# Kernel tuning notes

Hardware: AMD Instinct MI355X
Metric: run time of the kernel (lower is better)

The kernel has to match this reference:

```python
import jax, jax.numpy as jnp
import numpy as np

NUM_HEADS = 16
CAPACITY = 512
ROPE_BASE = 10000.0

def _rope_factor(positions, dim):
    # freqs = exp(linspace(0,-1,dim//2) * log(base)), shape (dim//2,)
    freqs = jnp.exp(jnp.linspace(0.0, -1.0, dim // 2) * jnp.log(jnp.float32(ROPE_BASE)))
    angles = positions[..., None] * freqs            # (..., seq, dim//2)
    return jnp.concatenate([jnp.sin(angles), jnp.cos(angles)], axis=-1)  # (..., seq, dim)

def setup_inputs() -> dict:
    key = jax.random.key(0)
    ks = jax.random.split(key, 6)
    B, Sq, Skv, D = 4, 4096, 4096, 1024
    return {
        "query_seq": jax.random.normal(ks[0], (B, Sq, D), jnp.float32),
        "value_seq": jax.random.normal(ks[1], (B, Skv, D), jnp.float32),
        "router_w": jax.random.normal(ks[2], (1, D), jnp.float32) * 0.02,
        "q_w": jax.random.normal(ks[3], (D, D), jnp.float32) * 0.02,
        "kv_w": jax.random.normal(ks[4], (2 * D, D), jnp.float32) * 0.02,
        "out_w": jax.random.normal(ks[5], (D, D), jnp.float32) * 0.02,
    }

def reference(query_seq, value_seq, router_w, q_w, kv_w, out_w):
    B, Sq, D = query_seq.shape
    Skv = value_seq.shape[1]
    H, C = NUM_HEADS, CAPACITY
    d = D // H

    # router + top-k capacity selection over the sequence dim
    rw = jnp.einsum("bsd,od->bs", query_seq, router_w).astype(jnp.float32)  # (B,Sq)
    top_w, top_idx = jax.lax.top_k(rw, C)                                   # (B,C)

    # gather selected queries
    resampled = jnp.take_along_axis(query_seq, top_idx[:, :, None], axis=1)  # (B,C,D)

    q = jnp.einsum("bcd,ed->bce", resampled, q_w)        # (B,C,H*d)
    kv = jnp.einsum("bsd,ed->bse", value_seq, kv_w)      # (B,Skv,2*H*d)
    k, v = jnp.split(kv, 2, axis=-1)

    q = q.reshape(B, C, H, d).transpose(0, 2, 1, 3)      # (B,H,C,d)
    k = k.reshape(B, Skv, H, d).transpose(0, 2, 1, 3)    # (B,H,Skv,d)
    v = v.reshape(B, Skv, H, d).transpose(0, 2, 1, 3)

    # RoPE-style elementwise modulation (faithful to source: x * cat(sin, cos))
    q_pos = top_idx.astype(jnp.float32)[:, None, :]      # (B,1,C)
    q = q * _rope_factor(q_pos, d)                       # (B,H,C,d)
    k_pos = jnp.arange(Skv, dtype=jnp.float32)[None, :]  # (1,Skv)
    k = k * _rope_factor(k_pos, d)[None]                 # broadcast over (B,H)

    # SDPA
    scores = jnp.einsum("bhcd,bhsd->bhcs", q, k) / jnp.sqrt(jnp.float32(d))
    att = jnp.einsum("bhcs,bhsd->bhcd", jax.nn.softmax(scores, axis=-1), v)

    att = att.transpose(0, 2, 1, 3).reshape(B, C, H * d)  # (B,C,D)
    att = jnp.einsum("bce,de->bcd", att, out_w)           # (B,C,D)

    # weighted scatter back to full sequence
    src = att * top_w[:, :, None]
    out = jnp.zeros_like(query_seq).at[jnp.arange(B)[:, None], top_idx].set(src)
    return out
```

## Files before the change

### kernel.cpp

```cpp
#include <hip/hip_runtime.h>
#include <hip/hip_bf16.h>

#define B_  4
#define SQ  4096
#define SKV 4096
#define DM  1024
#define NH  16
#define HD  64
#define CAP 512

#define ASPLIT 4
#define KVPER  (SKV / ASPLIT)
#define AITERS (KVPER / 64)

typedef __attribute__((ext_vector_type(8))) short    short8;
typedef __attribute__((ext_vector_type(8))) __bf16   bf16v8;
typedef __attribute__((ext_vector_type(4))) float    f32x4;
typedef __attribute__((ext_vector_type(4))) unsigned short ushort4v;
typedef __attribute__((ext_vector_type(4))) unsigned int   uint4v;

static __device__ __forceinline__ unsigned short f2bf(float f) {
    unsigned u = __float_as_uint(f);
    u += 0x7FFFu + ((u >> 16) & 1u);
    return (unsigned short)(u >> 16);
}

static __device__ __forceinline__ f32x4 mfma_bf16(short8 a, short8 b, f32x4 c) {
    return __builtin_amdgcn_mfma_f32_16x16x32_bf16(
        __builtin_bit_cast(bf16v8, a), __builtin_bit_cast(bf16v8, b), c, 0, 0, 0);
}

#define GLD16(gp, lp)                                                              \
    __builtin_amdgcn_global_load_lds(                                              \
        (__attribute__((address_space(1))) void*)(gp),                             \
        (__attribute__((address_space(3))) void*)(lp), 16, 0, 0)

__global__ void __launch_bounds__(256) k_convert(const float* __restrict__ in,
                                                 unsigned short* __restrict__ out) {
    size_t i = (size_t)blockIdx.x * 256 + threadIdx.x;
    float4 f = ((const float4*)in)[i];
    ushort4v o = { f2bf(f.x), f2bf(f.y), f2bf(f.z), f2bf(f.w) };
    ((ushort4v*)out)[i] = o;
}

__global__ void __launch_bounds__(256) k_rope(float* __restrict__ tab) {
    int g = blockIdx.x * 256 + threadIdx.x;
    int pos = g >> 6, i = g & 63, j = i & 31;
    float freq = expf(-(float)j * (logf(10000.0f) / 31.0f));
    float ang  = (float)pos * freq;
    tab[g] = (i < 32) ? sinf(ang) : cosf(ang);
}

__global__ void __launch_bounds__(256) k_router(const float* __restrict__ q,
                                                const float* __restrict__ wv,
                                                float* __restrict__ rw) {
    int row  = blockIdx.x * 4 + (threadIdx.x >> 6);
    int lane = threadIdx.x & 63;
    const float* p  = q  + (size_t)row * DM + lane * 16;
    const float* wp = wv + lane * 16;
    float s = 0.f;
#pragma unroll
    for (int j = 0; j < 4; j++) {
        float4 a = ((const float4*)p)[j];
        float4 b = ((const float4*)wp)[j];
        s += a.x * b.x + a.y * b.y + a.z * b.z + a.w * b.w;
    }
#pragma unroll
    for (int m = 32; m > 0; m >>= 1) s += __shfl_xor(s, m, 64);
    if (lane == 0) rw[row] = s;
}

__global__ void __launch_bounds__(1024) k_topk(const float* __restrict__ rw,
                                               int* __restrict__ sel,
                                               float* __restrict__ selw) {
    __shared__ unsigned long long keys[4096];
    int b = blockIdx.x, t = threadIdx.x;
    for (int i = t; i < 4096; i += 1024) {
        float v = rw[b * 4096 + i];
        unsigned u = __float_as_uint(v);
        u = (u & 0x80000000u) ? ~u : (u | 0x80000000u);
        keys[i] = ((unsigned long long)(~u) << 32) | (unsigned)i;
    }
    __syncthreads();
    for (int k = 2; k <= 4096; k <<= 1)
        for (int j = k >> 1; j > 0; j >>= 1) {
            for (int i = t; i < 4096; i += 1024) {
                int ixj = i ^ j;
                if (ixj > i) {
                    bool up = ((i & k) == 0);
                    unsigned long long a = keys[i], c = keys[ixj];
                    if ((a > c) == up) { keys[i] = c; keys[ixj] = a; }
                }
            }
            __syncthreads();
        }
    for (int i = t; i < 512; i += 1024) {
        unsigned idx = (unsigned)(keys[i] & 0xFFFFFFFFu);
        sel[b * 512 + i]  = (int)idx;
        selw[b * 512 + i] = rw[b * 4096 + idx];
    }
}

__global__ void __launch_bounds__(256) k_gather(const float* __restrict__ q,
                                                const int* __restrict__ sel,
                                                unsigned short* __restrict__ out) {
    int row = blockIdx.x;
    int b = row >> 9;
    int s = sel[row];
    const float4* src = (const float4*)(q + ((size_t)b * SQ + s) * DM);
    ushort4v* dst = (ushort4v*)(out + (size_t)row * DM);
    float4 f = src[threadIdx.x];
    ushort4v o = { f2bf(f.x), f2bf(f.y), f2bf(f.z), f2bf(f.w) };
    dst[threadIdx.x] = o;
}

template <int MODE, int BN>
__global__ void __launch_bounds__(256) k_gemm(
    const unsigned short* __restrict__ A,
    const unsigned short* __restrict__ Bw,
    int M, int N, int K,
    const float* __restrict__ rope_tab,
    const int* __restrict__ sel,
    const float* __restrict__ selw,
    unsigned short* __restrict__ ok,
    unsigned short* __restrict__ ov,
    unsigned short* __restrict__ obf,
    float* __restrict__ of) {
    constexpr int TN = BN / 32;
    __shared__ unsigned short lA[128 * 32];
    __shared__ unsigned short lB[BN * 32];
    const int tid = threadIdx.x;
    const int w = tid >> 6, lane = tid & 63, quad = lane >> 4, l16 = lane & 15;
    const int wr = w >> 1, wc = w & 1;
    const int mBase = blockIdx.y * 128;
    const int nBase = blockIdx.x * BN + (MODE == 3 ? 1024 : 0);

    f32x4 acc[4][TN] = {};

    for (int k0 = 0; k0 < K; k0 += 32) {
#pragma unroll
        for (int is = 0; is < 2; is++) {
            int slot = is * 256 + tid;
            int row = slot >> 2, sc = slot & 3;
            int kc = (sc - (row >> 1)) & 3;
            const char* ga = (const char*)A + (((size_t)(mBase + row) * K) + k0 + kc * 8) * 2;
            GLD16(ga, (char*)lA + slot * 16);
        }
#pragma unroll
        for (int is = 0; is < BN / 64; is++) {
            int slot = is * 256 + tid;
            int row = slot >> 2, sc = slot & 3;
            int kc = (sc - (row >> 1)) & 3;
            const char* gb = (const char*)Bw + (((size_t)(nBase + row) * K) + k0 + kc * 8) * 2;
            GLD16(gb, (char*)lB + slot * 16);
        }
        __syncthreads();
        short8 af[4], bfr[TN];
#pragma unroll
        for (int t = 0; t < 4; t++) {
            int r = wr * 64 + t * 16 + l16;
            af[t] = *(const short8*)&lA[r * 32 + (((quad + (r >> 1)) & 3) * 8)];
        }
#pragma unroll
        for (int t = 0; t < TN; t++) {
            int r = wc * (BN / 2) + t * 16 + l16;
            bfr[t] = *(const short8*)&lB[r * 32 + (((quad + (r >> 1)) & 3) * 8)];
        }
#pragma unroll
        for (int tm = 0; tm < 4; tm++)
#pragma unroll
            for (int tn = 0; tn < TN; tn++) {
                if constexpr (MODE == 3)
                    acc[tm][tn] = mfma_bf16(bfr[tn], af[tm], acc[tm][tn]);
                else
                    acc[tm][tn] = mfma_bf16(af[tm], bfr[tn], acc[tm][tn]);
            }
        __syncthreads();
    }

#pragma unroll
    for (int tm = 0; tm < 4; tm++) {
#pragma unroll
        for (int tn = 0; tn < TN; tn++) {
#pragma unroll
            for (int r = 0; r < 4; r++) {
                float v = acc[tm][tn][r];
                if constexpr (MODE == 3) {
                    int n = nBase + wc * (BN / 2) + tn * 16 + quad * 4 + r;
                    int m = mBase + wr * 64 + tm * 16 + l16;
                    int e = n - 1024, h = e >> 6, i = e & 63;
                    int b = m >> 12, s = m & 4095;
                    ov[(((size_t)(b * NH + h) * HD) + i) * SKV + s] = f2bf(v);
                } else {
                    int m = mBase + wr * 64 + tm * 16 + quad * 4 + r;
                    int n = nBase + wc * (BN / 2) + tn * 16 + l16;
                    if constexpr (MODE == 0) {
                        int b = m >> 12, s = m & 4095;
                        int h = n >> 6, i = n & 63;
                        v *= rope_tab[(s << 6) | i];
                        ok[(((size_t)(b * NH + h) * SKV) + s) * HD + i] = f2bf(v);
                    } else if constexpr (MODE == 1) {
                        int b = m >> 9, c = m & 511;
                        int h = n >> 6, i = n & 63;
                        float rp = rope_tab[(sel[m] << 6) | i];
                        obf[(((size_t)(b * NH + h) * CAP) + c) * HD + i] =
                            f2bf(v * rp * 0.18033688011112042f);
                    } else {
                        int b = m >> 9;
                        int s = sel[m];
                        of[(((size_t)b * SQ) + s) * DM + n] = v * selw[m];
                    }
                }
            }
        }
    }
}

__global__ void __launch_bounds__(256) k_attention(
    const unsigned short* __restrict__ Q,
    const unsigned short* __restrict__ Kg,
    const unsigned short* __restrict__ Vt,
    float* __restrict__ Opart,
    float* __restrict__ Lpart) {
    __shared__ unsigned short lK[64 * 72];
    __shared__ unsigned short lV[64 * 72];
    const int bh = blockIdx.y, z = blockIdx.z;
    const int tid = threadIdx.x, w = tid >> 6, lane = tid & 63;
    const int quad = lane >> 4, l16 = lane & 15;
    const int qb = blockIdx.x * 128 + w * 32;
    const int base = z * KVPER;

    short8 qf[2][2];
#pragma unroll
    for (int rt = 0; rt < 2; rt++) {
        const unsigned short* qp = Q + ((size_t)bh * CAP + qb + rt * 16 + l16) * HD + quad * 8;
        qf[rt][0] = *(const short8*)qp;
        qf[rt][1] = *(const short8*)(qp + 32);
    }

    const unsigned short* kb = Kg + (size_t)bh * SKV * HD;
    const unsigned short* vb = Vt + (size_t)bh * HD * SKV;
    const int sr = tid >> 2, sp = tid & 3;

    f32x4 o[2][4] = {};
    f32x4 lsum[2] = {};
    short8 ones = (short8)0x3F80;

    short8 rk0, rk1, rv0, rv1;
    {
        const short8* srck = (const short8*)(kb + (size_t)(base + sr) * HD + sp * 16);
        rk0 = srck[0]; rk1 = srck[1];
        const short8* srcv = (const short8*)(vb + (size_t)sr * SKV + base + sp * 16);
        rv0 = srcv[0]; rv1 = srcv[1];
    }

    for (int it = 0; it < AITERS; it++) {
        __syncthreads();
        *(short8*)&lK[sr * 72 + sp * 16]     = rk0;
        *(short8*)&lK[sr * 72 + sp * 16 + 8] = rk1;
        *(short8*)&lV[sr * 72 + sp * 16]     = rv0;
        *(short8*)&lV[sr * 72 + sp * 16 + 8] = rv1;
        if (it + 1 < AITERS) {
            int s0 = base + (it + 1) * 64;
            const short8* srck = (const short8*)(kb + (size_t)(s0 + sr) * HD + sp * 16);
            rk0 = srck[0]; rk1 = srck[1];
            const short8* srcv = (const short8*)(vb + (size_t)sr * SKV + s0 + sp * 16);
            rv0 = srcv[0]; rv1 = srcv[1];
        }
        __syncthreads();

        f32x4 sc[2][4] = {};
#pragma unroll
        for (int tn = 0; tn < 4; tn++) {
            short8 kf0 = *(const short8*)&lK[(tn * 16 + l16) * 72 + quad * 8];
            short8 kf1 = *(const short8*)&lK[(tn * 16 + l16) * 72 + 32 + quad * 8];
#pragma unroll
            for (int rt = 0; rt < 2; rt++) {
                sc[rt][tn] = mfma_bf16(kf0, qf[rt][0], sc[rt][tn]);
                sc[rt][tn] = mfma_bf16(kf1, qf[rt][1], sc[rt][tn]);
            }
        }
#pragma unroll
        for (int rt = 0; rt < 2; rt++)
#pragma unroll
            for (int tn = 0; tn < 4; tn++)
#pragma unroll
                for (int r = 0; r < 4; r++)
                    sc[rt][tn][r] = exp2f(fminf(sc[rt][tn][r], 86.f));

        short8 pa[2][2];
#pragma unroll
        for (int rt = 0; rt < 2; rt++)
#pragma unroll
            for (int kc = 0; kc < 2; kc++) {
                uint4v wv;
#pragma unroll
                for (int t = 0; t < 4; t++) {
                    unsigned pk;
                    asm("v_cvt_pk_bf16_f32 %0, %1, %2"
                        : "=v"(pk)
                        : "v"(sc[rt][kc * 2 + (t >> 1)][(t & 1) * 2]),
                          "v"(sc[rt][kc * 2 + (t >> 1)][(t & 1) * 2 + 1]));
                    wv[t] = pk;
                }
                pa[rt][kc] = __builtin_bit_cast(short8, wv);
            }

#pragma unroll
        for (int kc = 0; kc < 2; kc++) {
            lsum[0] = mfma_bf16(pa[0][kc], ones, lsum[0]);
            lsum[1] = mfma_bf16(pa[1][kc], ones, lsum[1]);
#pragma unroll
            for (int tn = 0; tn < 4; tn++) {
                const unsigned short* vrow = &lV[(size_t)(tn * 16 + l16) * 72];
                uint2 g0 = *(const uint2*)(vrow + kc * 32 + quad * 4);
                uint2 g1 = *(const uint2*)(vrow + kc * 32 + 16 + quad * 4);
                uint4v wv = { g0.x, g0.y, g1.x, g1.y };
                short8 vf = __builtin_bit_cast(short8, wv);
                o[0][tn] = mfma_bf16(pa[0][kc], vf, o[0][tn]);
                o[1][tn] = mfma_bf16(pa[1][kc], vf, o[1][tn]);
            }
        }
    }

    float* Ob = Opart + (((size_t)(z * 64 + bh)) * CAP + qb) * HD;
#pragma unroll
    for (int rt = 0; rt < 2; rt++)
#pragma unroll
        for (int tn = 0; tn < 4; tn++)
#pragma unroll
            for (int r = 0; r < 4; r++)
                Ob[(size_t)(rt * 16 + quad * 4 + r) * HD + tn * 16 + l16] = o[rt][tn][r];
    if (l16 == 0) {
#pragma unroll
        for (int rt = 0; rt < 2; rt++)
#pragma unroll
            for (int r = 0; r < 4; r++)
                Lpart[((size_t)(z * 64 + bh)) * CAP + qb + rt * 16 + quad * 4 + r] = lsum[rt][r];
    }
}

__global__ void __launch_bounds__(256) k_combine(
    const float* __restrict__ Opart, const float* __restrict__ Lpart,
    unsigned short* __restrict__ att) {
    int g = blockIdx.x * 256 + threadIdx.x;
    int dall = g & 1023, c = (g >> 10) & 511, b = g >> 19;
    int h = dall >> 6, dd = dall & 63;
    int bh = b * NH + h;
    float os = 0.f, ls = 0.f;
#pragma unroll
    for (int p = 0; p < ASPLIT; p++) {
        os += Opart[(((size_t)(p * 64 + bh)) * CAP + c) * HD + dd];
        ls += Lpart[((size_t)(p * 64 + bh)) * CAP + c];
    }
    att[g] = f2bf(os / ls);
}

extern "C" void kernel_launch(void* const* d_in, const int* in_sizes, int n_in,
                              void* d_out, int out_size, void* d_ws, size_t ws_size,
                              hipStream_t stream) {
    const float* query    = (const float*)d_in[0];
    const float* value    = (const float*)d_in[1];
    const float* router_w = (const float*)d_in[2];
    const float* q_w      = (const float*)d_in[3];
    const float* kv_w     = (const float*)d_in[4];
    const float* out_w    = (const float*)d_in[5];
    float* out = (float*)d_out;

    char* p = (char*)d_ws;
    unsigned short* value_bf = (unsigned short*)p; p += (size_t)B_ * SKV * DM * 2;
    unsigned short* kvw_bf   = (unsigned short*)p; p += (size_t)2 * DM * DM * 2;
    unsigned short* qw_bf    = (unsigned short*)p; p += (size_t)DM * DM * 2;
    unsigned short* ow_bf    = (unsigned short*)p; p += (size_t)DM * DM * 2;
    unsigned short* res_bf   = (unsigned short*)p; p += (size_t)B_ * CAP * DM * 2;
    unsigned short* q_attn   = (unsigned short*)p; p += (size_t)B_ * CAP * DM * 2;
    unsigned short* kbuf     = (unsigned short*)p; p += (size_t)B_ * SKV * DM * 2;
    unsigned short* vbuf     = (unsigned short*)p; p += (size_t)B_ * SKV * DM * 2;
    unsigned short* att_bf   = (unsigned short*)p; p += (size_t)B_ * CAP * DM * 2;
    float* rope_tab = (float*)p; p += (size_t)SKV * HD * 4;
    float* rw       = (float*)p; p += (size_t)B_ * SQ * 4;
    int*   sel      = (int*)p;   p += (size_t)B_ * CAP * 4;
    float* selw     = (float*)p; p += (size_t)B_ * CAP * 4;
    float* Opart = (float*)value_bf;
    float* Lpart = (float*)res_bf;

    hipMemsetAsync(d_out, 0, (size_t)out_size * sizeof(float), stream);

    k_convert<<<B_ * SKV * DM / 1024, 256, 0, stream>>>(value, value_bf);
    k_convert<<<2 * DM * DM / 1024, 256, 0, stream>>>(kv_w, kvw_bf);
    k_convert<<<DM * DM / 1024, 256, 0, stream>>>(q_w, qw_bf);
    k_convert<<<DM * DM / 1024, 256, 0, stream>>>(out_w, ow_bf);
    k_rope<<<SKV * HD / 256, 256, 0, stream>>>(rope_tab);
    k_router<<<B_ * SQ / 4, 256, 0, stream>>>(query, router_w, rw);
    k_topk<<<B_, 1024, 0, stream>>>(rw, sel, selw);
    k_gather<<<B_ * CAP, 256, 0, stream>>>(query, sel, res_bf);

    k_gemm<0, 128><<<dim3(DM / 128, B_ * SKV / 128), 256, 0, stream>>>(
        value_bf, kvw_bf, B_ * SKV, DM, DM, rope_tab, nullptr, nullptr,
        kbuf, nullptr, nullptr, nullptr);
    k_gemm<3, 128><<<dim3(DM / 128, B_ * SKV / 128), 256, 0, stream>>>(
        value_bf, kvw_bf, B_ * SKV, DM, DM, nullptr, nullptr, nullptr,
        nullptr, vbuf, nullptr, nullptr);
    k_gemm<1, 64><<<dim3(DM / 64, B_ * CAP / 128), 256, 0, stream>>>(
        res_bf, qw_bf, B_ * CAP, DM, DM, rope_tab, sel, nullptr,
        nullptr, nullptr, q_attn, nullptr);

    k_attention<<<dim3(CAP / 128, B_ * NH, ASPLIT), 256, 0, stream>>>(
        q_attn, kbuf, vbuf, Opart, Lpart);
    k_combine<<<B_ * CAP * DM / 256, 256, 0, stream>>>(Opart, Lpart, att_bf);

    k_gemm<2, 64><<<dim3(DM / 64, B_ * CAP / 128), 256, 0, stream>>>(
        att_bf, ow_bf, B_ * CAP, DM, DM, nullptr, sel, selw,
        nullptr, nullptr, nullptr, out);
}
```

Before: 483.6 us.

## Double-buffer attention K/V tiles and remap block IDs for L2 locality

The attention kernel now uses two LDS buffers for K and V, so the next tile is written while the current one is consumed. This cuts the barriers per iteration from two to one, and register prefetch now runs two tiles ahead. It also raises MFMA wave priority with s_setprio, drops the fminf clamp before exp2, and remaps workgroup IDs in both the GEMM and attention kernels in a chiplet/XCD-aware interleaved order to improve cache locality. The costs are double the LDS use and a possible overflow risk from removing the exp clamp.

```diff
diff --git a/kernel.cpp b/kernel.cpp
--- a/kernel.cpp
+++ b/kernel.cpp
@@ -127,13 +127,17 @@
     unsigned short* __restrict__ obf,
     float* __restrict__ of) {
     constexpr int TN = BN / 32;
+    constexpr int GX = DM / BN;
     __shared__ unsigned short lA[128 * 32];
     __shared__ unsigned short lB[BN * 32];
     const int tid = threadIdx.x;
     const int w = tid >> 6, lane = tid & 63, quad = lane >> 4, l16 = lane & 15;
     const int wr = w >> 1, wc = w & 1;
-    const int mBase = blockIdx.y * 128;
-    const int nBase = blockIdx.x * BN + (MODE == 3 ? 1024 : 0);
+    const int nwg = GX * (M >> 7);
+    const int bid0 = blockIdx.y * GX + blockIdx.x;
+    const int bid  = (bid0 & 7) * (nwg >> 3) + (bid0 >> 3);
+    const int mBase = (bid / GX) << 7;
+    const int nBase = (bid % GX) * BN + (MODE == 3 ? 1024 : 0);
 
     f32x4 acc[4][TN] = {};
 
@@ -216,18 +220,103 @@
     }
 }
 
+template <int C>
+static __device__ __forceinline__ void att_step(
+    int it, int base, int sr, int sp, int quad, int l16,
+    const unsigned short* __restrict__ kb, const unsigned short* __restrict__ vb,
+    unsigned short (*lK)[64 * 72], unsigned short (*lV)[64 * 72],
+    short8 (&rk)[2], short8 (&rv)[2],
+    const short8 (&qf)[2][2],
+    f32x4 (&o)[2][4], f32x4 (&lsum)[2], const short8 ones) {
+    if (it + 1 < AITERS) {
+        unsigned short* dK = &lK[C ^ 1][sr * 72 + sp * 16];
+        unsigned short* dV = &lV[C ^ 1][sr * 72 + sp * 16];
+        *(short8*)dK       = rk[0];
+        *(short8*)(dK + 8) = rk[1];
+        *(short8*)dV       = rv[0];
+        *(short8*)(dV + 8) = rv[1];
+    }
+    if (it + 2 < AITERS) {
+        int s0 = base + (it + 2) * 64;
+        const short8* srck = (const short8*)(kb + (size_t)(s0 + sr) * HD + sp * 16);
+        rk[0] = srck[0]; rk[1] = srck[1];
+        const short8* srcv = (const short8*)(vb + (size_t)sr * SKV + s0 + sp * 16);
+        rv[0] = srcv[0]; rv[1] = srcv[1];
+    }
+
+    f32x4 sc[2][4] = {};
+    __builtin_amdgcn_s_setprio(1);
+#pragma unroll
+    for (int tn = 0; tn < 4; tn++) {
+        short8 kf0 = *(const short8*)&lK[C][(tn * 16 + l16) * 72 + quad * 8];
+        short8 kf1 = *(const short8*)&lK[C][(tn * 16 + l16) * 72 + 32 + quad * 8];
+#pragma unroll
+        for (int rt = 0; rt < 2; rt++) {
+            sc[rt][tn] = mfma_bf16(kf0, qf[rt][0], sc[rt][tn]);
+            sc[rt][tn] = mfma_bf16(kf1, qf[rt][1], sc[rt][tn]);
+        }
+    }
+    __builtin_amdgcn_s_setprio(0);
+#pragma unroll
+    for (int rt = 0; rt < 2; rt++)
+#pragma unroll
+        for (int tn = 0; tn < 4; tn++)
+#pragma unroll
+            for (int r = 0; r < 4; r++)
+                sc[rt][tn][r] = exp2f(sc[rt][tn][r]);
+
+    short8 pa[2][2];
+#pragma unroll
+    for (int rt = 0; rt < 2; rt++)
+#pragma unroll
+        for (int kc = 0; kc < 2; kc++) {
+            uint4v wv;
+#pragma unroll
+            for (int t = 0; t < 4; t++) {
+                unsigned pk;
+                asm("v_cvt_pk_bf16_f32 %0, %1, %2"
+                    : "=v"(pk)
+                    : "v"(sc[rt][kc * 2 + (t >> 1)][(t & 1) * 2]),
+                      "v"(sc[rt][kc * 2 + (t >> 1)][(t & 1) * 2 + 1]));
+                wv[t] = pk;
+            }
+            pa[rt][kc] = __builtin_bit_cast(short8, wv);
+        }
+
+    __builtin_amdgcn_s_setprio(1);
+#pragma unroll
+    for (int kc = 0; kc < 2; kc++) {
+        lsum[0] = mfma_bf16(pa[0][kc], ones, lsum[0]);
+        lsum[1] = mfma_bf16(pa[1][kc], ones, lsum[1]);
+#pragma unroll
+        for (int tn = 0; tn < 4; tn++) {
+            const unsigned short* vrow = &lV[C][(size_t)(tn * 16 + l16) * 72];
+            uint2 g0 = *(const uint2*)(vrow + kc * 32 + quad * 4);
+            uint2 g1 = *(const uint2*)(vrow + kc * 32 + 16 + quad * 4);
+            uint4v wv = { g0.x, g0.y, g1.x, g1.y };
+            short8 vf = __builtin_bit_cast(short8, wv);
+            o[0][tn] = mfma_bf16(pa[0][kc], vf, o[0][tn]);
+            o[1][tn] = mfma_bf16(pa[1][kc], vf, o[1][tn]);
+        }
+    }
+    __builtin_amdgcn_s_setprio(0);
+    __syncthreads();
+}
+
 __global__ void __launch_bounds__(256) k_attention(
     const unsigned short* __restrict__ Q,
     const unsigned short* __restrict__ Kg,
     const unsigned short* __restrict__ Vt,
     float* __restrict__ Opart,
     float* __restrict__ Lpart) {
-    __shared__ unsigned short lK[64 * 72];
-    __shared__ unsigned short lV[64 * 72];
-    const int bh = blockIdx.y, z = blockIdx.z;
+    __shared__ unsigned short lK[2][64 * 72];
+    __shared__ unsigned short lV[2][64 * 72];
+    const int bid0 = (blockIdx.z * 64 + blockIdx.y) * 4 + blockIdx.x;
+    const int bid  = (bid0 & 7) * 128 + (bid0 >> 3);
+    const int bx = bid & 3, bh = (bid >> 2) & 63, z = bid >> 8;
     const int tid = threadIdx.x, w = tid >> 6, lane = tid & 63;
     const int quad = lane >> 4, l16 = lane & 15;
-    const int qb = blockIdx.x * 128 + w * 32;
+    const int qb = bx * 128 + w * 32;
     const int base = z * KVPER;
 
     short8 qf[2][2];
@@ -246,81 +335,33 @@
     f32x4 lsum[2] = {};
     short8 ones = (short8)0x3F80;
 
-    short8 rk0, rk1, rv0, rv1;
+    short8 rk[2], rv[2];
     {
         const short8* srck = (const short8*)(kb + (size_t)(base + sr) * HD + sp * 16);
-        rk0 = srck[0]; rk1 = srck[1];
+        rk[0] = srck[0]; rk[1] = srck[1];
         const short8* srcv = (const short8*)(vb + (size_t)sr * SKV + base + sp * 16);
-        rv0 = srcv[0]; rv1 = srcv[1];
-    }
-
-    for (int it = 0; it < AITERS; it++) {
-        __syncthreads();
-        *(short8*)&lK[sr * 72 + sp * 16]     = rk0;
-        *(short8*)&lK[sr * 72 + sp * 16 + 8] = rk1;
-        *(short8*)&lV[sr * 72 + sp * 16]     = rv0;
-        *(short8*)&lV[sr * 72 + sp * 16 + 8] = rv1;
-        if (it + 1 < AITERS) {
-            int s0 = base + (it + 1) * 64;
-            const short8* srck = (const short8*)(kb + (size_t)(s0 + sr) * HD + sp * 16);
-            rk0 = srck[0]; rk1 = srck[1];
-            const short8* srcv = (const short8*)(vb + (size_t)sr * SKV + s0 + sp * 16);
-            rv0 = srcv[0]; rv1 = srcv[1];
-        }
-        __syncthreads();
-
-        f32x4 sc[2][4] = {};
-#pragma unroll
-        for (int tn = 0; tn < 4; tn++) {
-            short8 kf0 = *(const short8*)&lK[(tn * 16 + l16) * 72 + quad * 8];
-            short8 kf1 = *(const short8*)&lK[(tn * 16 + l16) * 72 + 32 + quad * 8];
-#pragma unroll
-            for (int rt = 0; rt < 2; rt++) {
-                sc[rt][tn] = mfma_bf16(kf0, qf[rt][0], sc[rt][tn]);
-                sc[rt][tn] = mfma_bf16(kf1, qf[rt][1], sc[rt][tn]);
-            }
-        }
-#pragma unroll
-        for (int rt = 0; rt < 2; rt++)
-#pragma unroll
-            for (int tn = 0; tn < 4; tn++)
-#pragma unroll
-                for (int r = 0; r < 4; r++)
-                    sc[rt][tn][r] = exp2f(fminf(sc[rt][tn][r], 86.f));
-
-        short8 pa[2][2];
-#pragma unroll
-        for (int rt = 0; rt < 2; rt++)
-#pragma unroll
-            for (int kc = 0; kc < 2; kc++) {
-                uint4v wv;
-#pragma unroll
-                for (int t = 0; t < 4; t++) {
-                    unsigned pk;
-                    asm("v_cvt_pk_bf16_f32 %0, %1, %2"
-                        : "=v"(pk)
-                        : "v"(sc[rt][kc * 2 + (t >> 1)][(t & 1) * 2]),
-                          "v"(sc[rt][kc * 2 + (t >> 1)][(t & 1) * 2 + 1]));
-                    wv[t] = pk;
-                }
-                pa[rt][kc] = __builtin_bit_cast(short8, wv);
-            }
-
-#pragma unroll
-        for (int kc = 0; kc < 2; kc++) {
-            lsum[0] = mfma_bf16(pa[0][kc], ones, lsum[0]);
-            lsum[1] = mfma_bf16(pa[1][kc], ones, lsum[1]);
-#pragma unroll
-            for (int tn = 0; tn < 4; tn++) {
-                const unsigned short* vrow = &lV[(size_t)(tn * 16 + l16) * 72];
-                uint2 g0 = *(const uint2*)(vrow + kc * 32 + quad * 4);
-                uint2 g1 = *(const uint2*)(vrow + kc * 32 + 16 + quad * 4);
-                uint4v wv = { g0.x, g0.y, g1.x, g1.y };
-                short8 vf = __builtin_bit_cast(short8, wv);
-                o[0][tn] = mfma_bf16(pa[0][kc], vf, o[0][tn]);
-                o[1][tn] = mfma_bf16(pa[1][kc], vf, o[1][tn]);
-            }
-        }
+        rv[0] = srcv[0]; rv[1] = srcv[1];
+    }
+    {
+        unsigned short* dK = &lK[0][sr * 72 + sp * 16];
+        unsigned short* dV = &lV[0][sr * 72 + sp * 16];
+        *(short8*)dK       = rk[0];
+        *(short8*)(dK + 8) = rk[1];
+        *(short8*)dV       = rv[0];
+        *(short8*)(dV + 8) = rv[1];
+    }
+    {
+        int s0 = base + 64;
+        const short8* srck = (const short8*)(kb + (size_t)(s0 + sr) * HD + sp * 16);
+        rk[0] = srck[0]; rk[1] = srck[1];
+        const short8* srcv = (const short8*)(vb + (size_t)sr * SKV + s0 + sp * 16);
+        rv[0] = srcv[0]; rv[1] = srcv[1];
+    }
+    __syncthreads();
+
+    for (int it = 0; it < AITERS; it += 2) {
+        att_step<0>(it,     base, sr, sp, quad, l16, kb, vb, lK, lV, rk, rv, qf, o, lsum, ones);
+        att_step<1>(it + 1, base, sr, sp, quad, l16, kb, vb, lK, lV, rk, rv, qf, o, lsum, ones);
     }
 
     float* Ob = Opart + (((size_t)(z * 64 + bh)) * CAP + qb) * HD;
```

Result: faster. 461.9 us (-4.5%).
